# Performance work log

Measured on AMD Instinct MI355X. Metric: run time of the kernel, lower is better.

## Reference

```python
import jax, jax.numpy as jnp
import numpy as np

B, L, D, H, R = 4, 4096, 1024, 16, 30
DK = D // H  # 64
EPS = 1e-12  # torch F.normalize eps


def setup_inputs() -> dict:
    key = jax.random.key(0)
    ks = jax.random.split(key, 16)
    n = lambda k, shp, s=0.02: jax.random.normal(k, shp, jnp.float32) * s
    return {
        "queries": jax.random.normal(ks[0], (B, L, D), jnp.float32),
        "keys": jax.random.normal(ks[1], (B, L, D), jnp.float32),
        "values": jax.random.normal(ks[2], (B, L, D), jnp.float32),
        # linear weights stored as (in, out); equivalent to torch y = x @ W.T + b
        "Wq": n(ks[3], (D, D)), "bq": jnp.zeros((D,), jnp.float32),
        "Wk": n(ks[4], (D, D)), "bk": jnp.zeros((D,), jnp.float32),
        "We": n(ks[5], (H, DK, R), 0.1),
        "Wr": n(ks[6], (H, DK, R), 0.1),
        "Lam": jax.random.uniform(ks[7], (H, R), jnp.float32),
        "Wc": n(ks[8], (2 * R, DK)), "bc": jnp.zeros((DK,), jnp.float32),
        "Wo": n(ks[9], (D, D)), "bo": jnp.zeros((D,), jnp.float32),
    }


def _l2norm(x):
    nrm = jnp.sqrt(jnp.sum(x * x, axis=-1, keepdims=True))
    return x / jnp.maximum(nrm, EPS)


def reference(queries, keys, values, Wq, bq, Wk, bk, We, Wr, Lam, Wc, bc, Wo, bo):
    b, l, _ = queries.shape
    # projections -> [B, H, L, DK]
    q = (queries @ Wq + bq).reshape(b, l, H, DK).transpose(0, 2, 1, 3)
    k = (keys @ Wk + bk).reshape(b, l, H, DK).transpose(0, 2, 1, 3)
    # causal cumulative mean over sequence
    normal = (jnp.arange(l, dtype=jnp.float32) + 1.0)[None, None, :, None]
    q = jnp.cumsum(q, axis=2) / normal
    k = jnp.cumsum(k, axis=2) / normal
    # L2-normalized feature map
    q = _l2norm(q)
    k = _l2norm(k)
    # per-head low-rank projections -> [B, H, L, R]
    escore = jnp.einsum('bhld,hdr->bhlr', q, We)
    rscore = jnp.einsum('bhld,hdr->bhlr', k, Wr)
    score = jnp.concatenate([escore, rscore], axis=-1)  # [B, H, L, 2R]
    out = score @ Wc + bc                                # [B, H, L, DK]
    out = out.transpose(0, 2, 1, 3).reshape(b, l, H * DK)
    out = out @ Wo + bo                                  # [B, L, D]
    # dropout is identity in eval mode
    return (out, escore, rscore, Lam)
```

## Files before the change

kernel.cpp:

```cpp
#include <hip/hip_runtime.h>
#include <hip/hip_bf16.h>

#define BATCH 4
#define LSEQ 4096
#define DMODEL 1024
#define NHEAD 16
#define RDIM 30
#define DKH 64
#define NCHUNK 32
#define CHUNK 128

typedef __attribute__((ext_vector_type(8))) short bf16x8_t;
typedef __attribute__((ext_vector_type(4))) float f32x4_t;

static __device__ __forceinline__ unsigned short f2bf(float f) {
    __hip_bfloat16 h = __float2bfloat16(f);
    unsigned short u;
    __builtin_memcpy(&u, &h, 2);
    return u;
}
static __device__ __forceinline__ float b2f(unsigned short u) {
    unsigned v = ((unsigned)u) << 16;
    float f;
    __builtin_memcpy(&f, &v, 4);
    return f;
}

#define SWAIT_VM8()   { asm volatile("s_waitcnt vmcnt(8)" ::: "memory"); __builtin_amdgcn_sched_barrier(0); }
#define SWAIT_VM4()   { asm volatile("s_waitcnt vmcnt(4)" ::: "memory"); __builtin_amdgcn_sched_barrier(0); }
#define SWAIT_VM0()   { asm volatile("s_waitcnt vmcnt(0)" ::: "memory"); __builtin_amdgcn_sched_barrier(0); }
#define SWAIT_LGKM0() { asm volatile("s_waitcnt lgkmcnt(0)" ::: "memory"); __builtin_amdgcn_sched_barrier(0); }
#define SBARRIER()    { __builtin_amdgcn_s_barrier(); __builtin_amdgcn_sched_barrier(0); }

__global__ void transpose_cvt_kernel(const float* __restrict__ W0, const float* __restrict__ W1,
                                     unsigned short* __restrict__ O0, unsigned short* __restrict__ O1) {
    __shared__ float tile[32][33];
    const float* W = blockIdx.z ? W1 : W0;
    unsigned short* outT = blockIdx.z ? O1 : O0;
    int n0 = blockIdx.x * 32, k0 = blockIdx.y * 32;
    int tx = threadIdx.x, ty = threadIdx.y;
    #pragma unroll
    for (int r = ty; r < 32; r += 8)
        tile[r][tx] = W[(size_t)(k0 + r) * DMODEL + n0 + tx];
    __syncthreads();
    #pragma unroll
    for (int r = ty; r < 32; r += 8)
        outT[(size_t)(n0 + r) * DMODEL + k0 + tx] = f2bf(tile[tx][r]);
}

__global__ void wpack_kernel(const float* __restrict__ We, const float* __restrict__ Wr,
                             unsigned short* __restrict__ WeP, unsigned short* __restrict__ WrP) {
    int h = blockIdx.x;
    const float* W = blockIdx.y ? Wr : We;
    unsigned short* O = blockIdx.y ? WrP : WeP;
    for (int idx = threadIdx.x; idx < 2048; idx += 256) {
        int col = idx >> 6, k = idx & 63;
        float v = (col < RDIM) ? W[((size_t)h * 64 + k) * RDIM + col] : 0.f;
        O[((size_t)h << 11) + idx] = f2bf(v);
    }
}

__global__ __launch_bounds__(256) void wfold_kernel(
    const float* __restrict__ Wc, const float* __restrict__ Wo,
    unsigned short* __restrict__ WfoldT)
{
    __shared__ float WoT[64][65];
    __shared__ float WcT[64][61];
    const int tid = threadIdx.x;
    const int n0 = blockIdx.x * 64, h = blockIdx.y;
    for (int i = tid; i < 4096; i += 256) {
        int dk = i >> 6, n = i & 63;
        WoT[dk][n] = Wo[(size_t)(h * 64 + dk) * DMODEL + n0 + n];
    }
    for (int i = tid; i < 3840; i += 256) {
        int j = i >> 6, dk = i & 63;
        WcT[dk][j] = Wc[j * 64 + dk];
    }
    __syncthreads();
    #pragma unroll 1
    for (int oo = 0; oo < 16; ++oo) {
        int n = (tid >> 6) + oo * 4;
        int j = tid & 63;
        int jr = (j < 30) ? j : (j >= 32 && j < 62) ? (j - 2) : -1;
        float acc = 0.f;
        if (jr >= 0) {
            #pragma unroll
            for (int dk = 0; dk < 64; ++dk)
                acc = fmaf(WcT[dk][jr], WoT[dk][n], acc);
        }
        WfoldT[(size_t)(n0 + n) * 1024 + h * 64 + j] = f2bf(acc);
    }
}

__global__ void bias2_kernel(const float* __restrict__ Wo, const float* __restrict__ bc,
                             const float* __restrict__ bo, float* __restrict__ bias2) {
    int n = blockIdx.x * 256 + threadIdx.x;
    float a = bo[n];
    for (int d = 0; d < DMODEL; ++d)
        a = fmaf(bc[d & 63], Wo[(size_t)d * DMODEL + n], a);
    bias2[n] = a;
}

#define GBM 256
#define GBN 256
#define NTILES 16

template <bool AF32, bool BF16_OUT, bool DOCUM>
__global__ __launch_bounds__(512, 2) void gemm8_kernel(
    const void* __restrict__ Av0, const void* __restrict__ Av1,
    const unsigned short* __restrict__ Bt0, const unsigned short* __restrict__ Bt1,
    const float* __restrict__ bias0, const float* __restrict__ bias1,
    void* __restrict__ Cv0, void* __restrict__ Cv1,
    float* __restrict__ part0, float* __restrict__ part1,
    int N)
{
    __shared__ __align__(16) unsigned short As[2][GBM * 64];
    __shared__ __align__(16) unsigned short Bs[2][GBM * 64];
    const int tid = threadIdx.x;
    const int lane = tid & 63;
    const int wid = tid >> 6;
    const int wm = wid >> 2;
    const int wn = wid & 3;
    const int lm = lane & 15;
    const int kb = lane >> 4;
    const int z = blockIdx.z;

    const void* Av = z ? Av1 : Av0;
    const unsigned short* Bt = z ? Bt1 : Bt0;
    const float* bias = z ? bias1 : bias0;
    void* Cv = z ? Cv1 : Cv0;
    float* part = z ? part1 : part0;

    const int nwg = gridDim.x * gridDim.y;
    const int wg = blockIdx.y * gridDim.x + blockIdx.x;
    const int cpx = nwg >> 3;
    const int swz = (wg & 7) * cpx + (wg >> 3);
    const int bn = swz % gridDim.x;
    const int bm = swz / gridDim.x;

    const unsigned short* Btile = Bt + (size_t)(bn * GBN) * 1024;
    const float* A32_tile = nullptr;
    const unsigned short* A16_tile = nullptr;
    if constexpr (AF32) A32_tile = (const float*)Av + (size_t)(bm * GBM) * 1024;
    else                A16_tile = (const unsigned short*)Av + (size_t)(bm * GBM) * 1024;

    f32x4_t acc[8][4];
    #pragma unroll
    for (int i = 0; i < 8; ++i)
        #pragma unroll
        for (int j = 0; j < 4; ++j)
            acc[i][j] = f32x4_t{0.f, 0.f, 0.f, 0.f};

    auto B_STAGE = [&](int buf, int kt) {
        #pragma unroll
        for (int seg = 0; seg < 4; ++seg) {
            const int s = (seg << 13) + (tid << 4);
            const int row = s >> 7;
            const int cc = ((s >> 4) & 7) ^ (row & 7);
            const unsigned short* gb = Btile + (size_t)row * 1024 + kt * 64 + cc * 8;
            __builtin_amdgcn_global_load_lds(
                (const __attribute__((address_space(1))) void*)gb,
                (__attribute__((address_space(3))) void*)((char*)&Bs[buf][0] + (seg << 13) + (wid << 10)),
                16, 0, 0);
        }
    };
    auto A_STAGE16 = [&](int buf, int kt) {
        #pragma unroll
        for (int seg = 0; seg < 4; ++seg) {
            const int s = (seg << 13) + (tid << 4);
            const int row = s >> 7;
            const int cc = ((s >> 4) & 7) ^ (row & 7);
            const unsigned short* ga = A16_tile + (size_t)row * 1024 + kt * 64 + cc * 8;
            __builtin_amdgcn_global_load_lds(
                (const __attribute__((address_space(1))) void*)ga,
                (__attribute__((address_space(3))) void*)((char*)&As[buf][0] + (seg << 13) + (wid << 10)),
                16, 0, 0);
        }
    };
    float4 areg[8];
    auto A_ISSUE = [&](int kt) {
        #pragma unroll
        for (int p = 0; p < 8; ++p) {
            int q = p * 512 + tid;
            int row = q >> 4, kq = q & 15;
            areg[p] = *(const float4*)(A32_tile + (size_t)row * 1024 + kt * 64 + kq * 4);
        }
    };
    auto A_WRITE = [&](int buf) {
        #pragma unroll
        for (int p = 0; p < 8; ++p) {
            int q = p * 512 + tid;
            int row = q >> 4, kq = q & 15;
            ushort4 pk;
            pk.x = f2bf(areg[p].x); pk.y = f2bf(areg[p].y);
            pk.z = f2bf(areg[p].z); pk.w = f2bf(areg[p].w);
            int cc = (kq >> 1) ^ (row & 7);
            *(ushort4*)((char*)&As[buf][0] + row * 128 + (cc << 4) + (kq & 1) * 8) = pk;
        }
    };

    bf16x8_t af[8], bfr[4];
    auto LOADFRAGS = [&](int buf, int ks) {
        #pragma unroll
        for (int i = 0; i < 8; ++i) {
            int row = wm * 128 + i * 16 + lm;
            int cc = (ks * 4 + kb) ^ (row & 7);
            af[i] = *(const bf16x8_t*)((const char*)&As[buf][0] + row * 128 + cc * 16);
        }
        #pragma unroll
        for (int j = 0; j < 4; ++j) {
            int row = wn * 64 + j * 16 + lm;
            int cc = (ks * 4 + kb) ^ (row & 7);
            bfr[j] = *(const bf16x8_t*)((const char*)&Bs[buf][0] + row * 128 + cc * 16);
        }
    };
    auto MFMAC = [&]() {
        __builtin_amdgcn_s_setprio(1);
        #pragma unroll
        for (int i = 0; i < 8; ++i)
            #pragma unroll
            for (int j = 0; j < 4; ++j)
                acc[i][j] = __builtin_amdgcn_mfma_f32_16x16x32_bf16(af[i], bfr[j], acc[i][j], 0, 0, 0);
        __builtin_amdgcn_s_setprio(0);
    };

    if constexpr (AF32) {
        B_STAGE(0, 0);
        A_ISSUE(0);
        SWAIT_VM0();
        A_WRITE(0);
        B_STAGE(1, 1);
        A_ISSUE(1);
        SWAIT_LGKM0();
        SBARRIER();
    } else {
        A_STAGE16(0, 0);
        B_STAGE(0, 0);
        __builtin_amdgcn_sched_barrier(0);
        A_STAGE16(1, 1);
        B_STAGE(1, 1);
        SWAIT_VM8();
        SBARRIER();
    }

    int cur = 0;
    for (int t = 0; t < NTILES; ++t) {
        LOADFRAGS(cur, 0);
        MFMAC();
        LOADFRAGS(cur, 1);
        SWAIT_LGKM0();
        SBARRIER();
        if constexpr (AF32) {
            if (t + 2 < NTILES) B_STAGE(cur, t + 2);
            if (t + 1 < NTILES) {
                if (t + 2 < NTILES) { SWAIT_VM4(); }
                else                { SWAIT_VM0(); }
                A_WRITE(cur ^ 1);
                if (t + 2 < NTILES) A_ISSUE(t + 2);
            }
            MFMAC();
            if (t + 1 < NTILES) { SWAIT_LGKM0(); SBARRIER(); }
        } else {
            if (t + 2 < NTILES) { A_STAGE16(cur, t + 2); B_STAGE(cur, t + 2); }
            MFMAC();
            if (t + 1 < NTILES) {
                if (t + 2 < NTILES) { SWAIT_VM8(); }
                else                { SWAIT_VM0(); }
                SBARRIER();
            }
        }
        cur ^= 1;
    }

    if constexpr (DOCUM) {
        const int g = lane >> 4;
        const int row0 = bm * GBM + wm * 128;
        #pragma unroll
        for (int j = 0; j < 4; ++j) {
            const int col = bn * GBN + wn * 64 + j * 16 + lm;
            const float bv = bias[col];
            float runbase = 0.f;
            #pragma unroll
            for (int i = 0; i < 8; ++i) {
                float c0 = acc[i][j][0] + bv;
                float c1 = c0 + acc[i][j][1] + bv;
                float c2 = c1 + acc[i][j][2] + bv;
                float c3 = c2 + acc[i][j][3] + bv;
                float tot = c3;
                float x16 = __shfl_xor(tot, 16);
                float x32 = __shfl_xor(tot, 32);
                float x48 = __shfl_xor(x16, 32);
                float pre = (g == 1) ? x16
                          : (g == 2) ? (x32 + x48)
                          : (g == 3) ? (x16 + x32 + x48) : 0.f;
                float base2 = runbase + pre;
                runbase += tot + x16 + x32 + x48;
                int row = row0 + i * 16 + g * 4;
                unsigned short* cp = (unsigned short*)Cv + (size_t)row * N + col;
                cp[0]         = f2bf(base2 + c0);
                cp[(size_t)N] = f2bf(base2 + c1);
                cp[(size_t)2 * N] = f2bf(base2 + c2);
                cp[(size_t)3 * N] = f2bf(base2 + c3);
            }
            if (g == 0)
                part[((size_t)(row0 >> 7) << 10) + col] = runbase;
        }
    } else {
        #pragma unroll
        for (int i = 0; i < 8; ++i) {
            int row = bm * GBM + wm * 128 + i * 16 + (lane >> 4) * 4;
            #pragma unroll
            for (int j = 0; j < 4; ++j) {
                int col = bn * GBN + wn * 64 + j * 16 + lm;
                float bv = bias[col];
                #pragma unroll
                for (int r = 0; r < 4; ++r) {
                    float v = acc[i][j][r] + bv;
                    if constexpr (BF16_OUT)
                        ((unsigned short*)Cv)[(size_t)(row + r) * N + col] = f2bf(v);
                    else
                        ((float*)Cv)[(size_t)(row + r) * N + col] = v;
                }
            }
        }
    }
}

__global__ void chunk_offsets_kernel(float* __restrict__ partQ, float* __restrict__ partK)
{
    int t = blockIdx.x * 256 + threadIdx.x;
    float* part = blockIdx.y ? partK : partQ;
    int b = t >> 10, d = t & 1023;
    float run = 0.f;
    #pragma unroll
    for (int c = 0; c < NCHUNK; ++c) {
        size_t idx = ((size_t)(b * NCHUNK + c)) * DMODEL + d;
        float v = part[idx];
        part[idx] = run;
        run += v;
    }
}

__global__ __launch_bounds__(256) void score_kernel(
    const unsigned short* __restrict__ Qc, const unsigned short* __restrict__ Kc,
    const float* __restrict__ partQ, const float* __restrict__ partK,
    const unsigned short* __restrict__ WeP, const unsigned short* __restrict__ WrP,
    float* __restrict__ escore, float* __restrict__ rscore,
    unsigned short* __restrict__ sbf)
{
    __shared__ float n2buf[4][64];
    const int tid = threadIdx.x;
    const int lane = tid & 63;
    const int w = tid >> 6;
    const int lm = lane & 15;
    const int lk = lane >> 4;
    const int c = blockIdx.x;
    const int bh = blockIdx.y;
    const int z = blockIdx.z;
    const int b = bh >> 4, h = bh & 15;
    const unsigned short* X = z ? Kc : Qc;
    const float* part = z ? partK : partQ;
    const unsigned short* WP = z ? WrP : WeP;
    float* eout = z ? rscore : escore;
    const int row0 = c * 256 + w * 64;
    const int co = c * 2 + (w >> 1);

    const float* offp = part + ((size_t)(b * NCHUNK + co)) * DMODEL + h * 64 + lk * 8;
    float o0[8], o1[8];
    {
        float4 a = *(const float4*)(offp);
        float4 bb = *(const float4*)(offp + 4);
        float4 cc = *(const float4*)(offp + 32);
        float4 dd = *(const float4*)(offp + 36);
        o0[0] = a.x; o0[1] = a.y; o0[2] = a.z; o0[3] = a.w;
        o0[4] = bb.x; o0[5] = bb.y; o0[6] = bb.z; o0[7] = bb.w;
        o1[0] = cc.x; o1[1] = cc.y; o1[2] = cc.z; o1[3] = cc.w;
        o1[4] = dd.x; o1[5] = dd.y; o1[6] = dd.z; o1[7] = dd.w;
    }

    const unsigned short* wpb = WP + ((size_t)h << 11) + lm * 64 + lk * 8;
    bf16x8_t b00 = *(const bf16x8_t*)(wpb);
    bf16x8_t b01 = *(const bf16x8_t*)(wpb + 32);
    bf16x8_t b10 = *(const bf16x8_t*)(wpb + 16 * 64);
    bf16x8_t b11 = *(const bf16x8_t*)(wpb + 16 * 64 + 32);

    f32x4_t acc[4][2];
    float n2p[4];
    #pragma unroll
    for (int i = 0; i < 4; ++i) {
        n2p[i] = 0.f;
        acc[i][0] = f32x4_t{0.f, 0.f, 0.f, 0.f};
        acc[i][1] = f32x4_t{0.f, 0.f, 0.f, 0.f};
    }

    const unsigned short* xbase = X + ((size_t)(b * LSEQ + row0 + lm)) * DMODEL + h * 64 + lk * 8;
    #pragma unroll
    for (int i = 0; i < 4; ++i) {
        const unsigned short* xp = xbase + (size_t)(16 * i) * DMODEL;
        bf16x8_t x0 = *(const bf16x8_t*)(xp);
        bf16x8_t x1 = *(const bf16x8_t*)(xp + 32);
        bf16x8_t xa0, xa1;
        #pragma unroll
        for (int j = 0; j < 8; ++j) {
            float xf = b2f((unsigned short)x0[j]) + o0[j];
            n2p[i] = fmaf(xf, xf, n2p[i]);
            xa0[j] = (short)f2bf(xf);
        }
        #pragma unroll
        for (int j = 0; j < 8; ++j) {
            float xf = b2f((unsigned short)x1[j]) + o1[j];
            n2p[i] = fmaf(xf, xf, n2p[i]);
            xa1[j] = (short)f2bf(xf);
        }
        acc[i][0] = __builtin_amdgcn_mfma_f32_16x16x32_bf16(xa0, b00, acc[i][0], 0, 0, 0);
        acc[i][1] = __builtin_amdgcn_mfma_f32_16x16x32_bf16(xa0, b10, acc[i][1], 0, 0, 0);
        acc[i][0] = __builtin_amdgcn_mfma_f32_16x16x32_bf16(xa1, b01, acc[i][0], 0, 0, 0);
        acc[i][1] = __builtin_amdgcn_mfma_f32_16x16x32_bf16(xa1, b11, acc[i][1], 0, 0, 0);
    }

    #pragma unroll
    for (int i = 0; i < 4; ++i) {
        n2p[i] += __shfl_xor(n2p[i], 16);
        n2p[i] += __shfl_xor(n2p[i], 32);
    }
    if (lane < 16) {
        #pragma unroll
        for (int i = 0; i < 4; ++i) n2buf[w][16 * i + lane] = n2p[i];
    }
    __syncthreads();

    #pragma unroll
    for (int i = 0; i < 4; ++i) {
        f32x4_t n2v = *(const f32x4_t*)&n2buf[w][16 * i + lk * 4];
        float inv[4];
        #pragma unroll
        for (int r = 0; r < 4; ++r) {
            int lr = row0 + 16 * i + lk * 4 + r;
            inv[r] = 1.f / fmaxf(sqrtf(n2v[r]), 1e-12f * (float)(lr + 1));
        }
        #pragma unroll
        for (int j = 0; j < 2; ++j) {
            int col = 16 * j + lm;
            #pragma unroll
            for (int r = 0; r < 4; ++r) {
                int lr = row0 + 16 * i + lk * 4 + r;
                float v = acc[i][j][r] * inv[r];
                if (col < RDIM)
                    eout[(((size_t)(b * NHEAD + h)) * LSEQ + lr) * RDIM + col] = v;
                sbf[((size_t)(b * LSEQ + lr)) * 1024 + h * 64 + z * 32 + col] =
                    (col < RDIM) ? f2bf(v) : (unsigned short)0;
            }
        }
    }
}

extern "C" void kernel_launch(void* const* d_in, const int* in_sizes, int n_in,
                              void* d_out, int out_size, void* d_ws, size_t ws_size,
                              hipStream_t stream)
{
    const float* queries = (const float*)d_in[0];
    const float* keys    = (const float*)d_in[1];
    const float* Wq = (const float*)d_in[3];
    const float* bq = (const float*)d_in[4];
    const float* Wk = (const float*)d_in[5];
    const float* bk = (const float*)d_in[6];
    const float* We = (const float*)d_in[7];
    const float* Wr = (const float*)d_in[8];
    const float* Lam = (const float*)d_in[9];
    const float* Wc = (const float*)d_in[10];
    const float* bc = (const float*)d_in[11];
    const float* Wo = (const float*)d_in[12];
    const float* bo = (const float*)d_in[13];

    float* out = (float*)d_out;
    float* escore = out + (size_t)16777216;
    float* rscore = out + (size_t)24641536;
    float* lam_out = out + (size_t)32505856;

    char* ws = (char*)d_ws;
    unsigned short* sbf = (unsigned short*)ws;
    unsigned short* Qb  = (unsigned short*)(ws + 33554432);
    unsigned short* Kb  = (unsigned short*)(ws + 67108864);
    unsigned short* WqT = (unsigned short*)(ws + 100663296);
    unsigned short* WkT = (unsigned short*)(ws + 102760448);
    unsigned short* WfT = (unsigned short*)(ws + 104857600);
    float* bias2 = (float*)(ws + 106954752);
    float* partQ = (float*)(ws + 106958848);
    float* partK = (float*)(ws + 107483136);
    unsigned short* WeP = (unsigned short*)(ws + 108007424);
    unsigned short* WrP = (unsigned short*)(ws + 108072960);

    dim3 tb(32, 8);
    transpose_cvt_kernel<<<dim3(32, 32, 2), tb, 0, stream>>>(Wq, Wk, WqT, WkT);
    wpack_kernel<<<dim3(16, 2), 256, 0, stream>>>(We, Wr, WeP, WrP);
    wfold_kernel<<<dim3(16, 16), 256, 0, stream>>>(Wc, Wo, WfT);
    bias2_kernel<<<4, 256, 0, stream>>>(Wo, bc, bo, bias2);

    gemm8_kernel<true, true, true><<<dim3(4, 64, 2), 512, 0, stream>>>(
        queries, keys, WqT, WkT, bq, bk, Qb, Kb, partQ, partK, 1024);

    chunk_offsets_kernel<<<dim3(16, 2), 256, 0, stream>>>(partQ, partK);

    score_kernel<<<dim3(16, 64, 2), 256, 0, stream>>>(Qb, Kb, partQ, partK, WeP, WrP,
                                                      escore, rscore, sbf);

    gemm8_kernel<false, false, false><<<dim3(4, 64, 1), 512, 0, stream>>>(
        sbf, sbf, WfT, WfT, bias2, bias2, out, out, nullptr, nullptr, 1024);

    hipMemcpyAsync(lam_out, Lam, 480 * sizeof(float), hipMemcpyDeviceToDevice, stream);
}
```

Baseline: 270.0 us.

## Compact score K dimension to 960, merge prep kernels, batch cumsum shuffles

The folded output GEMM now uses a K dimension of 960 (16 heads x 60 real score columns) instead of 1024 with zero padding, so the score buffer and folded weight are packed densely. This cuts the output GEMM's K loop from 16 to 15 tiles and removes the padded zero writes. The pack and bias kernels are merged into one launch, and the cumsum epilogue batches its cross-lane shuffles (two shuffles instead of three). The 960-wide rows change global alignment patterns for the async LDS loads (row stride 1920 bytes still 16-byte aligned).

```diff
diff --git a/kernel.cpp b/kernel.cpp
--- a/kernel.cpp
+++ b/kernel.cpp
@@ -48,15 +48,26 @@
         outT[(size_t)(n0 + r) * DMODEL + k0 + tx] = f2bf(tile[tx][r]);
 }
 
-__global__ void wpack_kernel(const float* __restrict__ We, const float* __restrict__ Wr,
-                             unsigned short* __restrict__ WeP, unsigned short* __restrict__ WrP) {
-    int h = blockIdx.x;
-    const float* W = blockIdx.y ? Wr : We;
-    unsigned short* O = blockIdx.y ? WrP : WeP;
-    for (int idx = threadIdx.x; idx < 2048; idx += 256) {
-        int col = idx >> 6, k = idx & 63;
-        float v = (col < RDIM) ? W[((size_t)h * 64 + k) * RDIM + col] : 0.f;
-        O[((size_t)h << 11) + idx] = f2bf(v);
+__global__ void wprep_kernel(const float* __restrict__ We, const float* __restrict__ Wr,
+                             unsigned short* __restrict__ WeP, unsigned short* __restrict__ WrP,
+                             const float* __restrict__ Wo, const float* __restrict__ bc,
+                             const float* __restrict__ bo, float* __restrict__ bias2) {
+    int bid = blockIdx.x;
+    if (bid < 32) {
+        int h = bid >> 1;
+        const float* W = (bid & 1) ? Wr : We;
+        unsigned short* O = (bid & 1) ? WrP : WeP;
+        for (int idx = threadIdx.x; idx < 2048; idx += 256) {
+            int col = idx >> 6, k = idx & 63;
+            float v = (col < RDIM) ? W[((size_t)h * 64 + k) * RDIM + col] : 0.f;
+            O[((size_t)h << 11) + idx] = f2bf(v);
+        }
+    } else {
+        int n = (bid - 32) * 256 + threadIdx.x;
+        float a = bo[n];
+        for (int d = 0; d < DMODEL; ++d)
+            a = fmaf(bc[d & 63], Wo[(size_t)d * DMODEL + n], a);
+        bias2[n] = a;
     }
 }
 
@@ -81,31 +92,20 @@
     for (int oo = 0; oo < 16; ++oo) {
         int n = (tid >> 6) + oo * 4;
         int j = tid & 63;
-        int jr = (j < 30) ? j : (j >= 32 && j < 62) ? (j - 2) : -1;
-        float acc = 0.f;
-        if (jr >= 0) {
+        if (j < 60) {
+            float acc = 0.f;
             #pragma unroll
             for (int dk = 0; dk < 64; ++dk)
-                acc = fmaf(WcT[dk][jr], WoT[dk][n], acc);
-        }
-        WfoldT[(size_t)(n0 + n) * 1024 + h * 64 + j] = f2bf(acc);
-    }
-}
-
-__global__ void bias2_kernel(const float* __restrict__ Wo, const float* __restrict__ bc,
-                             const float* __restrict__ bo, float* __restrict__ bias2) {
-    int n = blockIdx.x * 256 + threadIdx.x;
-    float a = bo[n];
-    for (int d = 0; d < DMODEL; ++d)
-        a = fmaf(bc[d & 63], Wo[(size_t)d * DMODEL + n], a);
-    bias2[n] = a;
+                acc = fmaf(WcT[dk][j], WoT[dk][n], acc);
+            WfoldT[(size_t)(n0 + n) * 960 + h * 60 + j] = f2bf(acc);
+        }
+    }
 }
 
 #define GBM 256
 #define GBN 256
-#define NTILES 16
-
-template <bool AF32, bool BF16_OUT, bool DOCUM>
+
+template <bool AF32, bool BF16_OUT, bool DOCUM, int KD>
 __global__ __launch_bounds__(512, 2) void gemm8_kernel(
     const void* __restrict__ Av0, const void* __restrict__ Av1,
     const unsigned short* __restrict__ Bt0, const unsigned short* __restrict__ Bt1,
@@ -114,6 +114,7 @@
     float* __restrict__ part0, float* __restrict__ part1,
     int N)
 {
+    constexpr int NT = KD / 64;
     __shared__ __align__(16) unsigned short As[2][GBM * 64];
     __shared__ __align__(16) unsigned short Bs[2][GBM * 64];
     const int tid = threadIdx.x;
@@ -138,11 +139,11 @@
     const int bn = swz % gridDim.x;
     const int bm = swz / gridDim.x;
 
-    const unsigned short* Btile = Bt + (size_t)(bn * GBN) * 1024;
+    const unsigned short* Btile = Bt + (size_t)(bn * GBN) * KD;
     const float* A32_tile = nullptr;
     const unsigned short* A16_tile = nullptr;
-    if constexpr (AF32) A32_tile = (const float*)Av + (size_t)(bm * GBM) * 1024;
-    else                A16_tile = (const unsigned short*)Av + (size_t)(bm * GBM) * 1024;
+    if constexpr (AF32) A32_tile = (const float*)Av + (size_t)(bm * GBM) * KD;
+    else                A16_tile = (const unsigned short*)Av + (size_t)(bm * GBM) * KD;
 
     f32x4_t acc[8][4];
     #pragma unroll
@@ -157,7 +158,7 @@
             const int s = (seg << 13) + (tid << 4);
             const int row = s >> 7;
             const int cc = ((s >> 4) & 7) ^ (row & 7);
-            const unsigned short* gb = Btile + (size_t)row * 1024 + kt * 64 + cc * 8;
+            const unsigned short* gb = Btile + (size_t)row * KD + kt * 64 + cc * 8;
             __builtin_amdgcn_global_load_lds(
                 (const __attribute__((address_space(1))) void*)gb,
                 (__attribute__((address_space(3))) void*)((char*)&Bs[buf][0] + (seg << 13) + (wid << 10)),
@@ -170,7 +171,7 @@
             const int s = (seg << 13) + (tid << 4);
             const int row = s >> 7;
             const int cc = ((s >> 4) & 7) ^ (row & 7);
-            const unsigned short* ga = A16_tile + (size_t)row * 1024 + kt * 64 + cc * 8;
+            const unsigned short* ga = A16_tile + (size_t)row * KD + kt * 64 + cc * 8;
             __builtin_amdgcn_global_load_lds(
                 (const __attribute__((address_space(1))) void*)ga,
                 (__attribute__((address_space(3))) void*)((char*)&As[buf][0] + (seg << 13) + (wid << 10)),
@@ -183,7 +184,7 @@
         for (int p = 0; p < 8; ++p) {
             int q = p * 512 + tid;
             int row = q >> 4, kq = q & 15;
-            areg[p] = *(const float4*)(A32_tile + (size_t)row * 1024 + kt * 64 + kq * 4);
+            areg[p] = *(const float4*)(A32_tile + (size_t)row * KD + kt * 64 + kq * 4);
         }
     };
     auto A_WRITE = [&](int buf) {
@@ -244,28 +245,28 @@
     }
 
     int cur = 0;
-    for (int t = 0; t < NTILES; ++t) {
+    for (int t = 0; t < NT; ++t) {
         LOADFRAGS(cur, 0);
         MFMAC();
         LOADFRAGS(cur, 1);
         SWAIT_LGKM0();
         SBARRIER();
         if constexpr (AF32) {
-            if (t + 2 < NTILES) B_STAGE(cur, t + 2);
-            if (t + 1 < NTILES) {
-                if (t + 2 < NTILES) { SWAIT_VM4(); }
-                else                { SWAIT_VM0(); }
+            if (t + 2 < NT) B_STAGE(cur, t + 2);
+            if (t + 1 < NT) {
+                if (t + 2 < NT) { SWAIT_VM4(); }
+                else            { SWAIT_VM0(); }
                 A_WRITE(cur ^ 1);
-                if (t + 2 < NTILES) A_ISSUE(t + 2);
+                if (t + 2 < NT) A_ISSUE(t + 2);
             }
             MFMAC();
-            if (t + 1 < NTILES) { SWAIT_LGKM0(); SBARRIER(); }
+            if (t + 1 < NT) { SWAIT_LGKM0(); SBARRIER(); }
         } else {
-            if (t + 2 < NTILES) { A_STAGE16(cur, t + 2); B_STAGE(cur, t + 2); }
+            if (t + 2 < NT) { A_STAGE16(cur, t + 2); B_STAGE(cur, t + 2); }
             MFMAC();
-            if (t + 1 < NTILES) {
-                if (t + 2 < NTILES) { SWAIT_VM8(); }
-                else                { SWAIT_VM0(); }
+            if (t + 1 < NT) {
+                if (t + 2 < NT) { SWAIT_VM8(); }
+                else            { SWAIT_VM0(); }
                 SBARRIER();
             }
         }
@@ -279,28 +280,31 @@
         for (int j = 0; j < 4; ++j) {
             const int col = bn * GBN + wn * 64 + j * 16 + lm;
             const float bv = bias[col];
+            float c0[8], c1[8], c2[8], c3[8], tot[8], x16[8], x32s[8];
+            #pragma unroll
+            for (int i = 0; i < 8; ++i) {
+                c0[i] = acc[i][j][0] + bv;
+                c1[i] = c0[i] + acc[i][j][1] + bv;
+                c2[i] = c1[i] + acc[i][j][2] + bv;
+                c3[i] = c2[i] + acc[i][j][3] + bv;
+                tot[i] = c3[i];
+            }
+            #pragma unroll
+            for (int i = 0; i < 8; ++i) x16[i] = __shfl_xor(tot[i], 16);
+            #pragma unroll
+            for (int i = 0; i < 8; ++i) x32s[i] = __shfl_xor(tot[i] + x16[i], 32);
             float runbase = 0.f;
             #pragma unroll
             for (int i = 0; i < 8; ++i) {
-                float c0 = acc[i][j][0] + bv;
-                float c1 = c0 + acc[i][j][1] + bv;
-                float c2 = c1 + acc[i][j][2] + bv;
-                float c3 = c2 + acc[i][j][3] + bv;
-                float tot = c3;
-                float x16 = __shfl_xor(tot, 16);
-                float x32 = __shfl_xor(tot, 32);
-                float x48 = __shfl_xor(x16, 32);
-                float pre = (g == 1) ? x16
-                          : (g == 2) ? (x32 + x48)
-                          : (g == 3) ? (x16 + x32 + x48) : 0.f;
+                float pre = ((g & 1) ? x16[i] : 0.f) + ((g & 2) ? x32s[i] : 0.f);
                 float base2 = runbase + pre;
-                runbase += tot + x16 + x32 + x48;
+                runbase += tot[i] + x16[i] + x32s[i];
                 int row = row0 + i * 16 + g * 4;
                 unsigned short* cp = (unsigned short*)Cv + (size_t)row * N + col;
-                cp[0]         = f2bf(base2 + c0);
-                cp[(size_t)N] = f2bf(base2 + c1);
-                cp[(size_t)2 * N] = f2bf(base2 + c2);
-                cp[(size_t)3 * N] = f2bf(base2 + c3);
+                cp[0]             = f2bf(base2 + c0[i]);
+                cp[(size_t)N]     = f2bf(base2 + c1[i]);
+                cp[(size_t)2 * N] = f2bf(base2 + c2[i]);
+                cp[(size_t)3 * N] = f2bf(base2 + c3[i]);
             }
             if (g == 0)
                 part[((size_t)(row0 >> 7) << 10) + col] = runbase;
@@ -445,10 +449,10 @@
             for (int r = 0; r < 4; ++r) {
                 int lr = row0 + 16 * i + lk * 4 + r;
                 float v = acc[i][j][r] * inv[r];
-                if (col < RDIM)
+                if (col < RDIM) {
                     eout[(((size_t)(b * NHEAD + h)) * LSEQ + lr) * RDIM + col] = v;
-                sbf[((size_t)(b * LSEQ + lr)) * 1024 + h * 64 + z * 32 + col] =
-                    (col < RDIM) ? f2bf(v) : (unsigned short)0;
+                    sbf[((size_t)(b * LSEQ + lr)) * 960 + h * 60 + z * 30 + col] = f2bf(v);
+                }
             }
         }
     }
@@ -492,11 +496,10 @@
 
     dim3 tb(32, 8);
     transpose_cvt_kernel<<<dim3(32, 32, 2), tb, 0, stream>>>(Wq, Wk, WqT, WkT);
-    wpack_kernel<<<dim3(16, 2), 256, 0, stream>>>(We, Wr, WeP, WrP);
+    wprep_kernel<<<36, 256, 0, stream>>>(We, Wr, WeP, WrP, Wo, bc, bo, bias2);
     wfold_kernel<<<dim3(16, 16), 256, 0, stream>>>(Wc, Wo, WfT);
-    bias2_kernel<<<4, 256, 0, stream>>>(Wo, bc, bo, bias2);
-
-    gemm8_kernel<true, true, true><<<dim3(4, 64, 2), 512, 0, stream>>>(
+
+    gemm8_kernel<true, true, true, 1024><<<dim3(4, 64, 2), 512, 0, stream>>>(
         queries, keys, WqT, WkT, bq, bk, Qb, Kb, partQ, partK, 1024);
 
     chunk_offsets_kernel<<<dim3(16, 2), 256, 0, stream>>>(partQ, partK);
@@ -504,7 +507,7 @@
     score_kernel<<<dim3(16, 64, 2), 256, 0, stream>>>(Qb, Kb, partQ, partK, WeP, WrP,
                                                       escore, rscore, sbf);
 
-    gemm8_kernel<false, false, false><<<dim3(4, 64, 1), 512, 0, stream>>>(
+    gemm8_kernel<false, false, false, 960><<<dim3(4, 64, 1), 512, 0, stream>>>(
         sbf, sbf, WfT, WfT, bias2, bias2, out, out, nullptr, nullptr, 1024);
 
     hipMemcpyAsync(lam_out, Lam, 480 * sizeof(float), hipMemcpyDeviceToDevice, stream);
```

New measurement: 277.8 us. 2.9% more time.
